# Performance work log

Measured on AMD Instinct MI355X. Metric: run time of the kernel, lower is better.

## Reference

```python
import jax, jax.numpy as jnp
import numpy as np

INT_STEPS = 7  # scaling-and-squaring steps (module default)


def _warp(vol, flow):
    """Trilinear sample of vol at (identity grid + flow), border-clipped.
    vol, flow: [D, H, W, 3] -> [D, H, W, 3].
    """
    D, H, W, _ = vol.shape
    grid = jnp.stack(
        jnp.meshgrid(jnp.arange(D), jnp.arange(H), jnp.arange(W), indexing='ij'),
        axis=-1).astype(vol.dtype)
    maxs = jnp.array([D - 1, H - 1, W - 1], dtype=vol.dtype)
    loc = jnp.clip(grid + flow, 0.0, maxs)
    loc0 = jnp.floor(loc)
    w1 = loc - loc0          # weight of the upper corner along each axis
    w0 = 1.0 - w1
    i0 = loc0.astype(jnp.int32)
    i1 = jnp.minimum(i0 + 1, maxs.astype(jnp.int32))
    out = jnp.zeros_like(vol)
    for cx in (0, 1):
        for cy in (0, 1):
            for cz in (0, 1):
                ix = (i1 if cx else i0)[..., 0]
                iy = (i1 if cy else i0)[..., 1]
                iz = (i1 if cz else i0)[..., 2]
                w = ((w1 if cx else w0)[..., 0]
                     * (w1 if cy else w0)[..., 1]
                     * (w1 if cz else w0)[..., 2])
                out = out + w[..., None] * vol[ix, iy, iz]
    return out


def _integrate(vel):
    # scaling and squaring: v <- v + warp(v, v), repeated INT_STEPS times
    v = vel / (2.0 ** INT_STEPS)
    def body(_, v):
        return v + _warp(v, v)
    return jax.lax.fori_loop(0, INT_STEPS, body, v)


def setup_inputs() -> dict:
    key = jax.random.key(0)
    vel = jax.random.normal(key, (2, 128, 128, 128, 3), dtype=jnp.float32)
    return {"vel": vel}


def reference(vel):
    # indexing='ij' => no channel swap; vmap over batch (replaces tf.map_fn)
    return jax.vmap(_integrate)(vel)
```

## Files before the change

### kernel.cpp

```cpp
#include <hip/hip_runtime.h>


#define NVOX_PER_B (1 << 21)

typedef _Float16 h16;
typedef __attribute__((ext_vector_type(4))) _Float16 h16x4;

__device__ __forceinline__ void tri_setup(
    int x, int y, int z, float fx, float fy, float fz,
    int* off, float* w)
{
    float lx = fminf(fmaxf((float)x + fx, 0.0f), 127.0f);
    float ly = fminf(fmaxf((float)y + fy, 0.0f), 127.0f);
    float lz = fminf(fmaxf((float)z + fz, 0.0f), 127.0f);

    float flx = floorf(lx), fly = floorf(ly), flz = floorf(lz);
    float wx1 = lx - flx, wy1 = ly - fly, wz1 = lz - flz;
    float wx0 = 1.0f - wx1, wy0 = 1.0f - wy1, wz0 = 1.0f - wz1;

    int x0 = (int)flx, y0 = (int)fly, z0 = (int)flz;
    int x1 = min(x0 + 1, 127);
    int y1 = min(y0 + 1, 127);
    int z1 = min(z0 + 1, 127);

    off[0] = (x0 << 14) + (y0 << 7) + z0;
    off[1] = (x0 << 14) + (y0 << 7) + z1;
    off[2] = (x0 << 14) + (y1 << 7) + z0;
    off[3] = (x0 << 14) + (y1 << 7) + z1;
    off[4] = (x1 << 14) + (y0 << 7) + z0;
    off[5] = (x1 << 14) + (y0 << 7) + z1;
    off[6] = (x1 << 14) + (y1 << 7) + z0;
    off[7] = (x1 << 14) + (y1 << 7) + z1;
    w[0] = wx0 * wy0 * wz0;  w[1] = wx0 * wy0 * wz1;
    w[2] = wx0 * wy1 * wz0;  w[3] = wx0 * wy1 * wz1;
    w[4] = wx1 * wy0 * wz0;  w[5] = wx1 * wy0 * wz1;
    w[6] = wx1 * wy1 * wz0;  w[7] = wx1 * wy1 * wz1;
}

__device__ __forceinline__ void sample_h4(
    const h16x4* __restrict__ vb, const int* off, const float* w,
    float& ox, float& oy, float& oz)
{
    ox = 0.0f; oy = 0.0f; oz = 0.0f;
#pragma unroll
    for (int c = 0; c < 8; ++c) {
        h16x4 cv = vb[off[c]];
        ox += w[c] * (float)cv.x;
        oy += w[c] * (float)cv.y;
        oz += w[c] * (float)cv.z;
    }
}

__global__ __launch_bounds__(256) void vecint_first(
    const float* __restrict__ vin, h16x4* __restrict__ vout,
    float scale, int nvox)
{
    int idx = blockIdx.x * blockDim.x + threadIdx.x;
    if (idx >= nvox) return;

    int z = idx & 127;
    int y = (idx >> 7) & 127;
    int x = (idx >> 14) & 127;
    int b = idx >> 21;

    int base = idx * 3;
    float fx = vin[base + 0] * scale;
    float fy = vin[base + 1] * scale;
    float fz = vin[base + 2] * scale;

    int off[8]; float w[8];
    tri_setup(x, y, z, fx, fy, fz, off, w);

    const float* vb = vin + (size_t)b * (NVOX_PER_B * 3);
    float ox = 0.0f, oy = 0.0f, oz = 0.0f;
#pragma unroll
    for (int c = 0; c < 8; ++c) {
        const float* p = vb + (size_t)off[c] * 3;
        ox += w[c] * p[0]; oy += w[c] * p[1]; oz += w[c] * p[2];
    }

    h16x4 o;
    o.x = (h16)(fx + scale * ox);
    o.y = (h16)(fy + scale * oy);
    o.z = (h16)(fz + scale * oz);
    o.w = (h16)0.0f;
    vout[idx] = o;
}

__global__ __launch_bounds__(256) void vecint_mid(
    const h16x4* __restrict__ vin, h16x4* __restrict__ vout, int nvox)
{
    int idx = blockIdx.x * blockDim.x + threadIdx.x;
    if (idx >= nvox) return;

    int z = idx & 127;
    int y = (idx >> 7) & 127;
    int x = (idx >> 14) & 127;
    int b = idx >> 21;

    h16x4 f = vin[idx];
    float fx = (float)f.x, fy = (float)f.y, fz = (float)f.z;

    int off[8]; float w[8];
    tri_setup(x, y, z, fx, fy, fz, off, w);

    const h16x4* vb = vin + ((size_t)b << 21);
    float ox, oy, oz;
    sample_h4(vb, off, w, ox, oy, oz);

    h16x4 o;
    o.x = (h16)(fx + ox);
    o.y = (h16)(fy + oy);
    o.z = (h16)(fz + oz);
    o.w = (h16)0.0f;
    vout[idx] = o;
}

__global__ __launch_bounds__(256) void vecint_last(
    const h16x4* __restrict__ vin, float* __restrict__ vout, int nvox)
{
    int idx = blockIdx.x * blockDim.x + threadIdx.x;
    if (idx >= nvox) return;

    int z = idx & 127;
    int y = (idx >> 7) & 127;
    int x = (idx >> 14) & 127;
    int b = idx >> 21;

    h16x4 f = vin[idx];
    float fx = (float)f.x, fy = (float)f.y, fz = (float)f.z;

    int off[8]; float w[8];
    tri_setup(x, y, z, fx, fy, fz, off, w);

    const h16x4* vb = vin + ((size_t)b << 21);
    float ox, oy, oz;
    sample_h4(vb, off, w, ox, oy, oz);

    int base = idx * 3;
    vout[base + 0] = fx + ox;
    vout[base + 1] = fy + oy;
    vout[base + 2] = fz + oz;
}

extern "C" void kernel_launch(void* const* d_in, const int* in_sizes, int n_in,
                              void* d_out, int out_size, void* d_ws, size_t ws_size,
                              hipStream_t stream) {
    const float* vel = (const float*)d_in[0];
    float* out = (float*)d_out;

    int nvox = in_sizes[0] / 3;
    int blocks = (nvox + 255) / 256;
    float s0 = 1.0f / 128.0f;

    h16x4* D = (h16x4*)d_out;
    h16x4* W = (h16x4*)d_ws;

    vecint_first<<<blocks, 256, 0, stream>>>(vel, D, s0, nvox);
    vecint_mid  <<<blocks, 256, 0, stream>>>(D, W, nvox);
    vecint_mid  <<<blocks, 256, 0, stream>>>(W, D, nvox);
    vecint_mid  <<<blocks, 256, 0, stream>>>(D, W, nvox);
    vecint_mid  <<<blocks, 256, 0, stream>>>(W, D, nvox);
    vecint_mid  <<<blocks, 256, 0, stream>>>(D, W, nvox);
    vecint_last <<<blocks, 256, 0, stream>>>(W, out, nvox);
}
```

Measured before the change: 290.1 us.

## Stage 3D halo tiles in LDS for middle warp steps with global fallback

The middle scaling-and-squaring kernels now load a 16x8x16 voxel tile plus a 2-voxel halo into shared memory. Each thread processes 8 voxels and gathers its trilinear corners from LDS when they fall inside the tile, otherwise it falls back to global loads. The aim is to replace scattered global gathers with on-chip reuse. The cost is halo overfetch (20x12x20 per 2048 voxels), a block-wide sync, about 38KB of LDS per block that limits occupancy, and a divergent fallback path.

New measurement: 309.1 us. +6.6%, slower.

```diff
diff --git a/kernel.cpp b/kernel.cpp
--- a/kernel.cpp
+++ b/kernel.cpp
@@ -6,9 +6,17 @@
 typedef _Float16 h16;
 typedef __attribute__((ext_vector_type(4))) _Float16 h16x4;
 
-__device__ __forceinline__ void tri_setup(
+#define TX 16
+#define TY 8
+#define TZ 16
+#define LX (TX + 4)
+#define LY (TY + 4)
+#define LZ (TZ + 4)
+#define LDS_N (LX * LY * LZ)
+
+__device__ __forceinline__ void tri_setup_idx(
     int x, int y, int z, float fx, float fy, float fz,
-    int* off, float* w)
+    int& x0, int& x1, int& y0, int& y1, int& z0, int& z1, float* w)
 {
     float lx = fminf(fmaxf((float)x + fx, 0.0f), 127.0f);
     float ly = fminf(fmaxf((float)y + fy, 0.0f), 127.0f);
@@ -18,39 +26,17 @@
     float wx1 = lx - flx, wy1 = ly - fly, wz1 = lz - flz;
     float wx0 = 1.0f - wx1, wy0 = 1.0f - wy1, wz0 = 1.0f - wz1;
 
-    int x0 = (int)flx, y0 = (int)fly, z0 = (int)flz;
-    int x1 = min(x0 + 1, 127);
-    int y1 = min(y0 + 1, 127);
-    int z1 = min(z0 + 1, 127);
-
-    off[0] = (x0 << 14) + (y0 << 7) + z0;
-    off[1] = (x0 << 14) + (y0 << 7) + z1;
-    off[2] = (x0 << 14) + (y1 << 7) + z0;
-    off[3] = (x0 << 14) + (y1 << 7) + z1;
-    off[4] = (x1 << 14) + (y0 << 7) + z0;
-    off[5] = (x1 << 14) + (y0 << 7) + z1;
-    off[6] = (x1 << 14) + (y1 << 7) + z0;
-    off[7] = (x1 << 14) + (y1 << 7) + z1;
+    x0 = (int)flx; y0 = (int)fly; z0 = (int)flz;
+    x1 = min(x0 + 1, 127);
+    y1 = min(y0 + 1, 127);
+    z1 = min(z0 + 1, 127);
+
     w[0] = wx0 * wy0 * wz0;  w[1] = wx0 * wy0 * wz1;
     w[2] = wx0 * wy1 * wz0;  w[3] = wx0 * wy1 * wz1;
     w[4] = wx1 * wy0 * wz0;  w[5] = wx1 * wy0 * wz1;
     w[6] = wx1 * wy1 * wz0;  w[7] = wx1 * wy1 * wz1;
 }
 
-__device__ __forceinline__ void sample_h4(
-    const h16x4* __restrict__ vb, const int* off, const float* w,
-    float& ox, float& oy, float& oz)
-{
-    ox = 0.0f; oy = 0.0f; oz = 0.0f;
-#pragma unroll
-    for (int c = 0; c < 8; ++c) {
-        h16x4 cv = vb[off[c]];
-        ox += w[c] * (float)cv.x;
-        oy += w[c] * (float)cv.y;
-        oz += w[c] * (float)cv.z;
-    }
-}
-
 __global__ __launch_bounds__(256) void vecint_first(
     const float* __restrict__ vin, h16x4* __restrict__ vout,
     float scale, int nvox)
@@ -68,8 +54,14 @@
     float fy = vin[base + 1] * scale;
     float fz = vin[base + 2] * scale;
 
-    int off[8]; float w[8];
-    tri_setup(x, y, z, fx, fy, fz, off, w);
+    int x0, x1, y0, y1, z0, z1; float w[8];
+    tri_setup_idx(x, y, z, fx, fy, fz, x0, x1, y0, y1, z0, z1, w);
+
+    int off[8];
+    off[0] = (x0 << 14) + (y0 << 7) + z0;  off[1] = (x0 << 14) + (y0 << 7) + z1;
+    off[2] = (x0 << 14) + (y1 << 7) + z0;  off[3] = (x0 << 14) + (y1 << 7) + z1;
+    off[4] = (x1 << 14) + (y0 << 7) + z0;  off[5] = (x1 << 14) + (y0 << 7) + z1;
+    off[6] = (x1 << 14) + (y1 << 7) + z0;  off[7] = (x1 << 14) + (y1 << 7) + z1;
 
     const float* vb = vin + (size_t)b * (NVOX_PER_B * 3);
     float ox = 0.0f, oy = 0.0f, oz = 0.0f;
@@ -87,8 +79,92 @@
     vout[idx] = o;
 }
 
-__global__ __launch_bounds__(256) void vecint_mid(
-    const h16x4* __restrict__ vin, h16x4* __restrict__ vout, int nvox)
+__global__ __launch_bounds__(256) void vecint_mid_lds(
+    const h16x4* __restrict__ vin, h16x4* __restrict__ vout)
+{
+    __shared__ h16x4 tile[LDS_N];
+
+    int bid = blockIdx.x;
+    int tz = bid & 7;
+    int ty = (bid >> 3) & 15;
+    int tx = (bid >> 7) & 7;
+    int b  = bid >> 10;
+    int X0 = tx * TX, Y0 = ty * TY, Z0 = tz * TZ;
+
+    const h16x4* vb = vin + ((size_t)b << 21);
+
+    for (int s = (int)threadIdx.x; s < LDS_N; s += 256) {
+        int lz = s % LZ;
+        int r  = s / LZ;
+        int ly = r % LY;
+        int lx = r / LY;
+        int gx = min(max(X0 - 2 + lx, 0), 127);
+        int gy = min(max(Y0 - 2 + ly, 0), 127);
+        int gz = min(max(Z0 - 2 + lz, 0), 127);
+        tile[s] = vb[(gx << 14) + (gy << 7) + gz];
+    }
+    __syncthreads();
+
+#pragma unroll
+    for (int j = 0; j < 8; ++j) {
+        int wv = (int)threadIdx.x + 256 * j;
+        int vz = wv & 15;
+        int vy = (wv >> 4) & 7;
+        int vx = wv >> 7;
+        int x = X0 + vx, y = Y0 + vy, z = Z0 + vz;
+
+        h16x4 f = tile[((vx + 2) * LY + (vy + 2)) * LZ + (vz + 2)];
+        float fx = (float)f.x, fy = (float)f.y, fz = (float)f.z;
+
+        int x0, x1, y0, y1, z0, z1; float w[8];
+        tri_setup_idx(x, y, z, fx, fy, fz, x0, x1, y0, y1, z0, z1, w);
+
+        int lx0 = x0 - X0 + 2, lx1 = x1 - X0 + 2;
+        int ly0 = y0 - Y0 + 2, ly1 = y1 - Y0 + 2;
+        int lz0 = z0 - Z0 + 2, lz1 = z1 - Z0 + 2;
+
+        float ox = 0.0f, oy = 0.0f, oz = 0.0f;
+        bool in_tile = (lx0 >= 0) & (lx1 < LX) & (ly0 >= 0) & (ly1 < LY)
+                     & (lz0 >= 0) & (lz1 < LZ);
+        if (in_tile) {
+            int r00 = (lx0 * LY + ly0) * LZ, r01 = (lx0 * LY + ly1) * LZ;
+            int r10 = (lx1 * LY + ly0) * LZ, r11 = (lx1 * LY + ly1) * LZ;
+            h16x4 c0 = tile[r00 + lz0], c1 = tile[r00 + lz1];
+            h16x4 c2 = tile[r01 + lz0], c3 = tile[r01 + lz1];
+            h16x4 c4 = tile[r10 + lz0], c5 = tile[r10 + lz1];
+            h16x4 c6 = tile[r11 + lz0], c7 = tile[r11 + lz1];
+            ox = w[0]*(float)c0.x + w[1]*(float)c1.x + w[2]*(float)c2.x + w[3]*(float)c3.x
+               + w[4]*(float)c4.x + w[5]*(float)c5.x + w[6]*(float)c6.x + w[7]*(float)c7.x;
+            oy = w[0]*(float)c0.y + w[1]*(float)c1.y + w[2]*(float)c2.y + w[3]*(float)c3.y
+               + w[4]*(float)c4.y + w[5]*(float)c5.y + w[6]*(float)c6.y + w[7]*(float)c7.y;
+            oz = w[0]*(float)c0.z + w[1]*(float)c1.z + w[2]*(float)c2.z + w[3]*(float)c3.z
+               + w[4]*(float)c4.z + w[5]*(float)c5.z + w[6]*(float)c6.z + w[7]*(float)c7.z;
+        } else {
+            int off[8];
+            off[0] = (x0 << 14) + (y0 << 7) + z0;  off[1] = (x0 << 14) + (y0 << 7) + z1;
+            off[2] = (x0 << 14) + (y1 << 7) + z0;  off[3] = (x0 << 14) + (y1 << 7) + z1;
+            off[4] = (x1 << 14) + (y0 << 7) + z0;  off[5] = (x1 << 14) + (y0 << 7) + z1;
+            off[6] = (x1 << 14) + (y1 << 7) + z0;  off[7] = (x1 << 14) + (y1 << 7) + z1;
+#pragma unroll
+            for (int c = 0; c < 8; ++c) {
+                h16x4 cv = vb[off[c]];
+                ox += w[c] * (float)cv.x;
+                oy += w[c] * (float)cv.y;
+                oz += w[c] * (float)cv.z;
+            }
+        }
+
+        h16x4 o;
+        o.x = (h16)(fx + ox);
+        o.y = (h16)(fy + oy);
+        o.z = (h16)(fz + oz);
+        o.w = (h16)0.0f;
+        vout[(b << 21) + (x << 14) + (y << 7) + z] = o;
+    }
+}
+
+__global__ __launch_bounds__(256) void vecint_last(
+    const h16x4* __restrict__ vin, float* __restrict__ vout, int nvox)
 {
     int idx = blockIdx.x * blockDim.x + threadIdx.x;
     if (idx >= nvox) return;
@@ -101,41 +177,24 @@
     h16x4 f = vin[idx];
     float fx = (float)f.x, fy = (float)f.y, fz = (float)f.z;
 
-    int off[8]; float w[8];
-    tri_setup(x, y, z, fx, fy, fz, off, w);
+    int x0, x1, y0, y1, z0, z1; float w[8];
+    tri_setup_idx(x, y, z, fx, fy, fz, x0, x1, y0, y1, z0, z1, w);
+
+    int off[8];
+    off[0] = (x0 << 14) + (y0 << 7) + z0;  off[1] = (x0 << 14) + (y0 << 7) + z1;
+    off[2] = (x0 << 14) + (y1 << 7) + z0;  off[3] = (x0 << 14) + (y1 << 7) + z1;
+    off[4] = (x1 << 14) + (y0 << 7) + z0;  off[5] = (x1 << 14) + (y0 << 7) + z1;
+    off[6] = (x1 << 14) + (y1 << 7) + z0;  off[7] = (x1 << 14) + (y1 << 7) + z1;
 
     const h16x4* vb = vin + ((size_t)b << 21);
-    float ox, oy, oz;
-    sample_h4(vb, off, w, ox, oy, oz);
-
-    h16x4 o;
-    o.x = (h16)(fx + ox);
-    o.y = (h16)(fy + oy);
-    o.z = (h16)(fz + oz);
-    o.w = (h16)0.0f;
-    vout[idx] = o;
-}
-
-__global__ __launch_bounds__(256) void vecint_last(
-    const h16x4* __restrict__ vin, float* __restrict__ vout, int nvox)
-{
-    int idx = blockIdx.x * blockDim.x + threadIdx.x;
-    if (idx >= nvox) return;
-
-    int z = idx & 127;
-    int y = (idx >> 7) & 127;
-    int x = (idx >> 14) & 127;
-    int b = idx >> 21;
-
-    h16x4 f = vin[idx];
-    float fx = (float)f.x, fy = (float)f.y, fz = (float)f.z;
-
-    int off[8]; float w[8];
-    tri_setup(x, y, z, fx, fy, fz, off, w);
-
-    const h16x4* vb = vin + ((size_t)b << 21);
-    float ox, oy, oz;
-    sample_h4(vb, off, w, ox, oy, oz);
+    float ox = 0.0f, oy = 0.0f, oz = 0.0f;
+#pragma unroll
+    for (int c = 0; c < 8; ++c) {
+        h16x4 cv = vb[off[c]];
+        ox += w[c] * (float)cv.x;
+        oy += w[c] * (float)cv.y;
+        oz += w[c] * (float)cv.z;
+    }
 
     int base = idx * 3;
     vout[base + 0] = fx + ox;
@@ -151,16 +210,17 @@
 
     int nvox = in_sizes[0] / 3;
     int blocks = (nvox + 255) / 256;
+    int tblocks = 2 * 8 * 16 * 8;
     float s0 = 1.0f / 128.0f;
 
     h16x4* D = (h16x4*)d_out;
     h16x4* W = (h16x4*)d_ws;
 
-    vecint_first<<<blocks, 256, 0, stream>>>(vel, D, s0, nvox);
-    vecint_mid  <<<blocks, 256, 0, stream>>>(D, W, nvox);
-    vecint_mid  <<<blocks, 256, 0, stream>>>(W, D, nvox);
-    vecint_mid  <<<blocks, 256, 0, stream>>>(D, W, nvox);
-    vecint_mid  <<<blocks, 256, 0, stream>>>(W, D, nvox);
-    vecint_mid  <<<blocks, 256, 0, stream>>>(D, W, nvox);
-    vecint_last <<<blocks, 256, 0, stream>>>(W, out, nvox);
-}
+    vecint_first  <<<blocks,  256, 0, stream>>>(vel, D, s0, nvox);
+    vecint_mid_lds<<<tblocks, 256, 0, stream>>>(D, W);
+    vecint_mid_lds<<<tblocks, 256, 0, stream>>>(W, D);
+    vecint_mid_lds<<<tblocks, 256, 0, stream>>>(D, W);
+    vecint_mid_lds<<<tblocks, 256, 0, stream>>>(W, D);
+    vecint_mid_lds<<<tblocks, 256, 0, stream>>>(D, W);
+    vecint_last   <<<blocks,  256, 0, stream>>>(W, out, nvox);
+}
```
